# Optimization experiments

Measured on AMD Instinct MI355X. Metric: run time of the kernel, lower is better.

Reference implementation:

```python
import jax, jax.numpy as jnp
import numpy as np
from itertools import combinations

WAY = 5
TSS = 3  # temporal_set_size


def setup_inputs() -> dict:
    key = jax.random.key(0)
    k1, k2, k3 = jax.random.split(key, 3)
    n_support, n_queries, seq_len, D = 25, 400, 8, 2048
    d_out = D // 2
    support_set = jax.random.normal(k1, (n_support, seq_len, D), dtype=jnp.float32)
    queries = jax.random.normal(k2, (n_queries, seq_len, D), dtype=jnp.float32)
    support_labels = jnp.arange(n_support, dtype=jnp.int64) % WAY  # shot=5 per class
    W = jax.random.normal(k3, (d_out, TSS * D), dtype=jnp.float32) * 0.02
    b = jnp.zeros((d_out,), dtype=jnp.float32)
    return {"support_set": support_set, "support_labels": support_labels,
            "queries": queries, "W": W, "b": b}


def reference(support_set, support_labels, queries, W, b):
    # Dropout is identity at inference; omitted for determinism.
    n_s, seq_len, D = support_set.shape
    n_q = queries.shape[0]
    tup = jnp.asarray(list(combinations(range(seq_len), TSS)))  # [Tn, 3]
    Tn = tup.shape[0]
    # gather frame tuples and flatten: [N, Tn, 3*D]
    s = support_set[:, tup, :].reshape(n_s, Tn, TSS * D)
    q = queries[:, tup, :].reshape(n_q, Tn, TSS * D)
    # Linear + ReLU embedding
    qe = jax.nn.relu(q.reshape(n_q * Tn, TSS * D) @ W.T + b)          # [Q*Tn, d2]
    se = jax.nn.relu(s.reshape(n_s * Tn, TSS * D) @ W.T + b)
    se = se.reshape(n_s, Tn, -1)
    # group support by class (labels are static ints; shot per class is equal)
    order = jnp.argsort(support_labels, stable=True)                  # sorted by label
    cls_se = se[order.reshape(WAY, -1)].reshape(WAY, -1, se.shape[-1])  # [way, shot*Tn, d2]
    # pairwise Euclidean distances per class: ||q||^2 + ||s||^2 - 2 q.s
    q2 = jnp.sum(qe * qe, axis=-1)                                    # [Q*Tn]
    s2 = jnp.sum(cls_se * cls_se, axis=-1)                            # [way, shot*Tn]
    dots = jnp.einsum('qd,csd->cqs', qe, cls_se)                      # [way, Q*Tn, shot*Tn]
    dist = jnp.sqrt(jnp.maximum(q2[None, :, None] + s2[:, None, :] - 2.0 * dots, 0.0))
    min_dist = dist.min(axis=2).reshape(WAY, n_q, Tn)                 # min over class supports
    logits = -min_dist.mean(axis=2).T                                 # [n_q, way]
    return logits
```

## Files before the change

### kernel.cpp

```cpp
#include <hip/hip_runtime.h>
#include <math.h>

#define NSUP 25
#define NQ   400
#define SL   8
#define DIM  2048
#define DOUT 1024
#define WAY  5
#define TN   56
#define SHOT 5
#define QT   (NQ*TN)
#define STC  (SHOT*TN)
#define NFS  (NSUP*SL)
#define NFQ  (NQ*SL)
#define MF   (NFS+NFQ)
#define MFP  3584
#define PN   (3*DOUT)
#define NSE  1400
#define NSEP 1408

typedef __attribute__((ext_vector_type(8))) short short8;
typedef __attribute__((ext_vector_type(8))) int   int8v;
typedef __attribute__((ext_vector_type(4))) float f32x4;

#define GLOAD_LDS(g, l) __builtin_amdgcn_global_load_lds( \
    (const __attribute__((address_space(1))) unsigned*)(g), \
    (__attribute__((address_space(3))) unsigned*)(l), 16, 0, 0)

__device__ __forceinline__ unsigned short f2bf(float x) {
  unsigned u = __float_as_uint(x);
  u += 0x7fff + ((u >> 16) & 1);
  return (unsigned short)(u >> 16);
}
__device__ __forceinline__ float bf2f(unsigned short h) {
  return __uint_as_float(((unsigned)h) << 16);
}
__device__ __forceinline__ unsigned pk4_fp8(float a, float b, float c, float d) {
  unsigned p = __builtin_amdgcn_cvt_pk_fp8_f32(a, b, 0, false);
  p = __builtin_amdgcn_cvt_pk_fp8_f32(c, d, p, true);
  return p;
}
__device__ __forceinline__ float f8deq(unsigned b) {
  unsigned e = (b >> 3) & 15, m = b & 7;
  return e ? ldexpf((float)(8 + m), (int)e - 10) : ldexpf((float)m, -9);
}

__device__ __constant__ unsigned short TUP[TN] = {
  0x210,0x310,0x410,0x510,0x610,0x710,
  0x320,0x420,0x520,0x620,0x720,
  0x430,0x530,0x630,0x730,
  0x540,0x640,0x740,
  0x650,0x750,
  0x760,
  0x321,0x421,0x521,0x621,0x721,
  0x431,0x531,0x631,0x731,
  0x541,0x641,0x741,
  0x651,0x751,
  0x761,
  0x432,0x532,0x632,0x732,
  0x542,0x642,0x742,
  0x652,0x752,
  0x762,
  0x543,0x643,0x743,
  0x653,0x753,
  0x763,
  0x654,0x754,
  0x764,
  0x765
};

__global__ __launch_bounds__(256) void prep(
    const float* __restrict__ sup, const float* __restrict__ qry,
    const float* __restrict__ W,
    unsigned char* __restrict__ A8, unsigned char* __restrict__ W8,
    unsigned char* __restrict__ se8, float* __restrict__ s2,
    unsigned* __restrict__ pmin)
{
  int idx = blockIdx.x * 256 + threadIdx.x;
  {
    int e = idx * 4;
    int row = e >> 11, c = e & 2047;
    float4 v = make_float4(0.f, 0.f, 0.f, 0.f);
    if (row < NFS)      v = *(const float4*)(sup + (size_t)row * DIM + c);
    else if (row < MF)  v = *(const float4*)(qry + (size_t)(row - NFS) * DIM + c);
    *(unsigned*)(A8 + e) = pk4_fp8(v.x, v.y, v.z, v.w);
  }
  if (idx < PN*DIM/4) {
    int e = idx * 4;
    int n = e >> 11, c = e & 2047;
    const float4 v = *(const float4*)(W + (size_t)(n & 1023) * (3*DIM) + (n >> 10) * DIM + c);
    *(unsigned*)(W8 + e) = pk4_fp8(v.x*64.f, v.y*64.f, v.z*64.f, v.w*64.f);
  }
  if (idx < WAY * QT) pmin[idx] = 0x7F800000u;
  if (idx < (NSEP - NSE) * DOUT) se8[(size_t)NSE * DOUT + idx] = 0;
  if (idx < NSEP - NSE) s2[NSE + idx] = 0.f;
}

__device__ __forceinline__ void mfma_kloop_f8(
    const unsigned char* __restrict__ gA, const unsigned char* __restrict__ gB,
    int sa, int sb, int rowA0, int rowB0, int clampA,
    unsigned char* As, unsigned char* Bs,
    int w, int l, int nk, f32x4 acc[8][4])
{
  const int lrow = l >> 3;
  const int cswz = ((((l >> 1) & 3) ^ (lrow & 3)) * 2 + (l & 1)) * 16;
  unsigned offA[8], offB[4];
#pragma unroll
  for (int q = 0; q < 8; ++q)
    offA[q] = (unsigned)min(rowA0 + w*64 + q*8 + lrow, clampA) * sa + cswz;
#pragma unroll
  for (int q = 0; q < 4; ++q)
    offB[q] = (unsigned)(rowB0 + w*32 + q*8 + lrow) * sb + cswz;
  unsigned char* lA = As + (w*64) * 128;
  unsigned char* lB = Bs + (w*32) * 128;
  const int lane15 = l & 15, quad = l >> 4;
  const int wm = (w & 1) * 128, wn = (w >> 1) * 64;
  const int slot = (quad ^ (lane15 & 3)) * 32;

  int koff = 0;
  for (int kk = 0; kk < nk; ++kk, koff += 128) {
    __syncthreads();
#pragma unroll
    for (int q = 0; q < 8; ++q) GLOAD_LDS(gA + offA[q] + koff, lA + q*1024);
#pragma unroll
    for (int q = 0; q < 4; ++q) GLOAD_LDS(gB + offB[q] + koff, lB + q*1024);
    __syncthreads();
    int8v af[8];
#pragma unroll
    for (int i = 0; i < 8; ++i)
      af[i] = *(const int8v*)(As + (wm + i*16 + lane15)*128 + slot);
#pragma unroll
    for (int j = 0; j < 4; ++j) {
      int8v bf = *(const int8v*)(Bs + (wn + j*16 + lane15)*128 + slot);
#pragma unroll
      for (int i = 0; i < 8; ++i)
        acc[i][j] = __builtin_amdgcn_mfma_scale_f32_16x16x128_f8f6f4(
            af[i], bf, acc[i][j], 0, 0, 0, 0x7f7f7f7f, 0, 0x7f7f7f7f);
    }
  }
}

__global__ __launch_bounds__(256, 2) void gemm_embed_f8(
    const unsigned char* __restrict__ A8, const unsigned char* __restrict__ W8,
    unsigned short* __restrict__ P)
{
  __shared__ unsigned char As[256*128];
  __shared__ unsigned char Bs[128*128];
  int n = blockIdx.x;
  int g = n / 112, j = n % 112;
  const int bm = (j >> 3) * 256, bn = (g*8 + (j & 7)) * 128;
  const int tid = threadIdx.x, w = tid >> 6, l = tid & 63;
  const int lane15 = l & 15, quad = l >> 4;
  const int wm = (w & 1) * 128, wn = (w >> 1) * 64;

  f32x4 acc[8][4] = {};
  mfma_kloop_f8(A8, W8, DIM, DIM, bm, bn, MFP-1, As, Bs, w, l, DIM/128, acc);

#pragma unroll
  for (int i = 0; i < 8; ++i) {
#pragma unroll
    for (int r = 0; r < 4; ++r) {
      int row = bm + wm + i*16 + quad*4 + r;
      if (row < MF) {
#pragma unroll
        for (int j2 = 0; j2 < 4; ++j2) {
          int col = bn + wn + j2*16 + lane15;
          P[(size_t)row * PN + col] = f2bf(acc[i][j2][r] * 0.015625f);
        }
      }
    }
  }
}

__global__ __launch_bounds__(256) void assemble_seq(
    const unsigned short* __restrict__ P, const float* __restrict__ bias,
    unsigned char* __restrict__ qe8, float* __restrict__ q2,
    unsigned char* __restrict__ se8, float* __restrict__ s2)
{
  __shared__ unsigned short sP[SL * PN];
  const int b2 = blockIdx.x, b = b2 >> 1, half = b2 & 1;
  const int tid = threadIdx.x, w = tid >> 6, l = tid & 63;

  const size_t base = (size_t)b * SL * PN;
#pragma unroll
  for (int qi = 0; qi < 12; ++qi) {
    int off = (qi * 256 + tid) * 8;
    *(short8*)&sP[off] = *(const short8*)(P + base + off);
  }
  __syncthreads();

  float4 bbv[4];
#pragma unroll
  for (int c = 0; c < 4; ++c)
    bbv[c] = *(const float4*)&bias[l*4 + c*256];

  const bool is_sup = b < NSUP;
  unsigned char* E = is_sup ? se8 : qe8;
  float* nrm = is_sup ? s2 : q2;
  int row_base;
  if (is_sup) { int cc = b % WAY, kk = b / WAY; row_base = cc * STC + kk * TN; }
  else        { row_base = (b - NSUP) * TN; }

  const int t_end = half * 28 + 28;
  for (int t = half * 28 + w; t < t_end; t += 4) {
    unsigned int tp = TUP[t];
    int f0 = tp & 15, f1 = (tp >> 4) & 15, f2 = (tp >> 8) & 15;
    int row = row_base + t;
    float ssq = 0.f;
#pragma unroll
    for (int c = 0; c < 4; ++c) {
      int o = l*4 + c*256;
      ushort4 a = *(const ushort4*)&sP[f0*PN + o];
      ushort4 bq = *(const ushort4*)&sP[f1*PN + DOUT + o];
      ushort4 d = *(const ushort4*)&sP[f2*PN + 2*DOUT + o];
      float z0 = fmaxf(bf2f(a.x) + bf2f(bq.x) + bf2f(d.x) + bbv[c].x, 0.f);
      float z1 = fmaxf(bf2f(a.y) + bf2f(bq.y) + bf2f(d.y) + bbv[c].y, 0.f);
      float z2 = fmaxf(bf2f(a.z) + bf2f(bq.z) + bf2f(d.z) + bbv[c].z, 0.f);
      float z3 = fmaxf(bf2f(a.w) + bf2f(bq.w) + bf2f(d.w) + bbv[c].w, 0.f);
      unsigned pk = pk4_fp8(z0, z1, z2, z3);
      *(unsigned*)&E[(size_t)row * DOUT + o] = pk;
      float x0 = f8deq(pk & 255),         x1 = f8deq((pk >> 8) & 255);
      float x2 = f8deq((pk >> 16) & 255), x3 = f8deq(pk >> 24);
      ssq += x0*x0 + x1*x1 + x2*x2 + x3*x3;
    }
#pragma unroll
    for (int off = 1; off < 64; off <<= 1) ssq += __shfl_xor(ssq, off, 64);
    if (l == 0) nrm[row] = ssq;
  }
}

__global__ __launch_bounds__(256, 2) void gemm_dist_f8(
    const unsigned char* __restrict__ qe8, const unsigned char* __restrict__ se8,
    const float* __restrict__ q2, const float* __restrict__ s2,
    unsigned* __restrict__ pmin)
{
  __shared__ unsigned char As[256*128];
  __shared__ unsigned char Bs[128*128];
  int n = blockIdx.x;
  int x, y;
  if (n < 1008) { int g = n / 48, j = n % 48; y = g*8 + (j & 7); x = j >> 3; }
  else          { int m = n - 1008; y = 168 + m % 7; x = m / 7; }
  const int bm = x * 256;
  const int bn = y * 128;
  const int tid = threadIdx.x, w = tid >> 6, l = tid & 63;
  const int lane15 = l & 15, quad = l >> 4;
  const int wm = (w & 1) * 128, wn = (w >> 1) * 64;

  f32x4 acc[8][4] = {};
  mfma_kloop_f8(se8, qe8, DOUT, DOUT, bm, bn, NSEP-1, As, Bs, w, l, DOUT/128, acc);

  float s2v[8][4]; int clsv[8][4];
#pragma unroll
  for (int i = 0; i < 8; ++i)
#pragma unroll
    for (int r = 0; r < 4; ++r) {
      int sec = bm + wm + i*16 + quad*4 + r;
      s2v[i][r] = s2[min(sec, NSEP-1)];
      clsv[i][r] = sec / STC;
    }
#pragma unroll
  for (int i = 0; i < 8; ++i)
#pragma unroll
    for (int j = 0; j < 4; ++j)
#pragma unroll
      for (int r = 0; r < 4; ++r)
        acc[i][j][r] = fmaf(-2.f, acc[i][j][r], s2v[i][r]);

  float q2v[4];
#pragma unroll
  for (int j = 0; j < 4; ++j)
    q2v[j] = q2[bn + wn + j*16 + lane15];

  const int c_lo = (bm + wm) / STC;
  const int c_hi = min((bm + wm + 127) / STC, WAY - 1);
  for (int c = c_lo; c <= c_hi; ++c) {
#pragma unroll
    for (int j = 0; j < 4; ++j) {
      float mv = INFINITY;
#pragma unroll
      for (int i = 0; i < 8; ++i)
#pragma unroll
        for (int r = 0; r < 4; ++r)
          mv = fminf(mv, (clsv[i][r] == c) ? acc[i][j][r] : INFINITY);
      mv = fminf(mv, __shfl_xor(mv, 16, 64));
      mv = fminf(mv, __shfl_xor(mv, 32, 64));
      if (quad == 0) {
        float val = fmaxf(q2v[j] + mv, 0.f);
        atomicMin(&pmin[(size_t)c * QT + bn + wn + j*16 + lane15],
                  __float_as_uint(val));
      }
    }
  }
}

__global__ void finalize(const unsigned* __restrict__ pmin, float* __restrict__ out)
{
  int idx = blockIdx.x * blockDim.x + threadIdx.x;
  if (idx >= NQ * WAY) return;
  int i = idx / WAY, c = idx % WAY;
  float sum = 0.f;
  for (int t = 0; t < TN; ++t) {
    float v = __uint_as_float(pmin[(size_t)c * QT + i * TN + t]);
    sum += sqrtf(v);
  }
  out[i * WAY + c] = -sum * (1.f / (float)TN);
}

extern "C" void kernel_launch(void* const* d_in, const int* in_sizes, int n_in,
                              void* d_out, int out_size, void* d_ws, size_t ws_size,
                              hipStream_t stream) {
  const float* support = (const float*)d_in[0];
  const float* queries  = (const float*)d_in[2];
  const float* W        = (const float*)d_in[3];
  const float* bias     = (const float*)d_in[4];
  float* out = (float*)d_out;

  char* ws = (char*)d_ws;
  unsigned char* A8 = (unsigned char*)ws;           ws += (size_t)MFP * DIM;
  unsigned char* W8 = (unsigned char*)ws;           ws += (size_t)PN * DIM;
  unsigned short* P = (unsigned short*)ws;          ws += (size_t)MF * PN * 2;
  unsigned char* qe8 = (unsigned char*)ws;          ws += (size_t)QT * DOUT;
  unsigned char* se8 = (unsigned char*)ws;          ws += (size_t)NSEP * DOUT;
  float*         q2  = (float*)ws;                  ws += (size_t)QT * 4;
  float*         s2  = (float*)ws;                  ws += (size_t)NSEP * 4;
  unsigned*      pm  = (unsigned*)ws;

  prep<<<MFP*DIM/4/256, 256, 0, stream>>>(support, queries, W, A8, W8, se8, s2, pm);
  gemm_embed_f8<<<336, 256, 0, stream>>>(A8, W8, P);
  assemble_seq<<<2*(NSUP + NQ), 256, 0, stream>>>(P, bias, qe8, q2, se8, s2);
  gemm_dist_f8<<<1050, 256, 0, stream>>>(qe8, se8, q2, s2, pm);
  finalize<<<(NQ*WAY + 255)/256, 256, 0, stream>>>(pm, out);
}
```

Measured before the change: 201.2 us.

## Fuse frame-embedding GEMM with tuple assembly, dropping the bf16 intermediate buffer

Merges the frame-level embedding GEMM and the tuple-assembly kernel into one kernel. Each block computes a 64-frame by 128-output-column slice across all three weight segments, stages it as bf16 in LDS, then builds the ReLU'd fp8 tuple embeddings and partial squared norms directly. Norms are accumulated with atomics into buffers that prep now zeroes. This removes the global write and re-read of the intermediate P buffer and one kernel launch. The cost is a smaller GEMM tile with less reuse, plus per-row atomics. The fp8 dequantisation helper is also rewritten as bit manipulation instead of ldexpf.

```diff
diff --git a/kernel.cpp b/kernel.cpp
--- a/kernel.cpp
+++ b/kernel.cpp
@@ -14,6 +14,7 @@
 #define NFS  (NSUP*SL)
 #define NFQ  (NQ*SL)
 #define MF   (NFS+NFQ)
+#define NSEQ (NSUP+NQ)
 #define MFP  3584
 #define PN   (3*DOUT)
 #define NSE  1400
@@ -42,7 +43,9 @@
 }
 __device__ __forceinline__ float f8deq(unsigned b) {
   unsigned e = (b >> 3) & 15, m = b & 7;
-  return e ? ldexpf((float)(8 + m), (int)e - 10) : ldexpf((float)m, -9);
+  float n = __uint_as_float(((e + 120) << 23) | (m << 20));
+  float s = (float)m * 0.001953125f;
+  return e ? n : s;
 }
 
 __device__ __constant__ unsigned short TUP[TN] = {
@@ -74,7 +77,7 @@
     const float* __restrict__ W,
     unsigned char* __restrict__ A8, unsigned char* __restrict__ W8,
     unsigned char* __restrict__ se8, float* __restrict__ s2,
-    unsigned* __restrict__ pmin)
+    float* __restrict__ q2, unsigned* __restrict__ pmin)
 {
   int idx = blockIdx.x * 256 + threadIdx.x;
   {
@@ -93,7 +96,113 @@
   }
   if (idx < WAY * QT) pmin[idx] = 0x7F800000u;
   if (idx < (NSEP - NSE) * DOUT) se8[(size_t)NSE * DOUT + idx] = 0;
-  if (idx < NSEP - NSE) s2[NSE + idx] = 0.f;
+  if (idx < QT)   q2[idx] = 0.f;
+  if (idx < NSEP) s2[idx] = 0.f;
+}
+
+__global__ __launch_bounds__(256, 2) void embed_fused(
+    const unsigned char* __restrict__ A8, const unsigned char* __restrict__ W8,
+    const float* __restrict__ bias,
+    unsigned char* __restrict__ qe8, float* __restrict__ q2,
+    unsigned char* __restrict__ se8, float* __restrict__ s2)
+{
+  __shared__ __align__(16) unsigned char smem[57344];
+  unsigned char* As = smem;
+  unsigned char* Bs = smem + 8192;
+  unsigned short* sPb = (unsigned short*)smem;
+
+  const int bid = blockIdx.x;
+  const int ot = bid & 7, bs = bid >> 3;
+  const int bm = bs * 64;
+  const int tid = threadIdx.x, w = tid >> 6, l = tid & 63;
+  const int lane15 = l & 15, quad = l >> 4;
+  const int lrow = l >> 3;
+  const int cswz = ((((l >> 1) & 3) ^ (lrow & 3)) * 2 + (l & 1)) * 16;
+
+  unsigned offA[2], offB[12];
+#pragma unroll
+  for (int q = 0; q < 2; ++q)
+    offA[q] = (unsigned)min(bm + w*16 + q*8 + lrow, MF-1) * DIM + cswz;
+#pragma unroll
+  for (int m = 0; m < 12; ++m) {
+    int s = m >> 2, q = m & 3;
+    offB[m] = (unsigned)(s*1024 + ot*128 + w*32 + q*8 + lrow) * DIM + cswz;
+  }
+  const int slot = (quad ^ (lane15 & 3)) * 32;
+
+  f32x4 acc[4][6] = {};
+  int koff = 0;
+  for (int kk = 0; kk < 16; ++kk, koff += 128) {
+    __syncthreads();
+#pragma unroll
+    for (int q = 0; q < 2; ++q)
+      GLOAD_LDS(A8 + offA[q] + koff, As + (w*16)*128 + q*1024);
+#pragma unroll
+    for (int m = 0; m < 12; ++m) {
+      int s = m >> 2, q = m & 3;
+      GLOAD_LDS(W8 + offB[m] + koff, Bs + (s*128 + w*32)*128 + q*1024);
+    }
+    __syncthreads();
+    int8v af[4];
+#pragma unroll
+    for (int i = 0; i < 4; ++i)
+      af[i] = *(const int8v*)(As + (i*16 + lane15)*128 + slot);
+#pragma unroll
+    for (int j = 0; j < 6; ++j) {
+      int8v bf = *(const int8v*)(Bs + (w*96 + j*16 + lane15)*128 + slot);
+#pragma unroll
+      for (int i = 0; i < 4; ++i)
+        acc[i][j] = __builtin_amdgcn_mfma_scale_f32_16x16x128_f8f6f4(
+            af[i], bf, acc[i][j], 0, 0, 0, 0x7f7f7f7f, 0, 0x7f7f7f7f);
+    }
+  }
+
+  __syncthreads();
+#pragma unroll
+  for (int i = 0; i < 4; ++i)
+#pragma unroll
+    for (int j = 0; j < 6; ++j)
+#pragma unroll
+      for (int r = 0; r < 4; ++r)
+        sPb[(i*16 + quad*4 + r)*384 + (w*96 + j*16 + lane15)] =
+            f2bf(acc[i][j][r] * 0.015625f);
+  __syncthreads();
+
+  const int sl = 2*w + (l >> 5);
+  const int lc = l & 31;
+  const int seq = bs*8 + sl;
+  const int og = ot*128 + lc*4;
+  const float4 bb = *(const float4*)&bias[og];
+  const bool valid = seq < NSEQ;
+  const bool is_sup = seq < NSUP;
+  unsigned char* E = is_sup ? se8 : qe8;
+  float* nrm = is_sup ? s2 : q2;
+  int row_base = is_sup ? (seq % WAY) * STC + (seq / WAY) * TN
+                        : (seq - NSUP) * TN;
+  const unsigned short* base0 = sPb + sl * 8 * 384 + lc * 4;
+
+  for (int t = 0; t < TN; ++t) {
+    unsigned tp = TUP[t];
+    int f0 = tp & 15, f1 = (tp >> 4) & 15, f2 = (tp >> 8) & 15;
+    ushort4 a  = *(const ushort4*)(base0 + f0*384);
+    ushort4 bq = *(const ushort4*)(base0 + f1*384 + 128);
+    ushort4 d  = *(const ushort4*)(base0 + f2*384 + 256);
+    float z0 = fmaxf(bf2f(a.x) + bf2f(bq.x) + bf2f(d.x) + bb.x, 0.f);
+    float z1 = fmaxf(bf2f(a.y) + bf2f(bq.y) + bf2f(d.y) + bb.y, 0.f);
+    float z2 = fmaxf(bf2f(a.z) + bf2f(bq.z) + bf2f(d.z) + bb.z, 0.f);
+    float z3 = fmaxf(bf2f(a.w) + bf2f(bq.w) + bf2f(d.w) + bb.w, 0.f);
+    unsigned pk = pk4_fp8(z0, z1, z2, z3);
+    float x0 = f8deq(pk & 255),         x1 = f8deq((pk >> 8) & 255);
+    float x2 = f8deq((pk >> 16) & 255), x3 = f8deq(pk >> 24);
+    float ssq = x0*x0 + x1*x1 + x2*x2 + x3*x3;
+#pragma unroll
+    for (int off = 1; off < 32; off <<= 1) ssq += __shfl_xor(ssq, off, 64);
+    if (valid) {
+      int row = row_base + t;
+      *(unsigned*)&E[(size_t)row * DOUT + og] = pk;
+      if (lc == 0) atomicAdd(&nrm[row], ssq);
+    }
+  }
 }
 
 __device__ __forceinline__ void mfma_kloop_f8(
@@ -137,95 +246,6 @@
         acc[i][j] = __builtin_amdgcn_mfma_scale_f32_16x16x128_f8f6f4(
             af[i], bf, acc[i][j], 0, 0, 0, 0x7f7f7f7f, 0, 0x7f7f7f7f);
     }
-  }
-}
-
-__global__ __launch_bounds__(256, 2) void gemm_embed_f8(
-    const unsigned char* __restrict__ A8, const unsigned char* __restrict__ W8,
-    unsigned short* __restrict__ P)
-{
-  __shared__ unsigned char As[256*128];
-  __shared__ unsigned char Bs[128*128];
-  int n = blockIdx.x;
-  int g = n / 112, j = n % 112;
-  const int bm = (j >> 3) * 256, bn = (g*8 + (j & 7)) * 128;
-  const int tid = threadIdx.x, w = tid >> 6, l = tid & 63;
-  const int lane15 = l & 15, quad = l >> 4;
-  const int wm = (w & 1) * 128, wn = (w >> 1) * 64;
-
-  f32x4 acc[8][4] = {};
-  mfma_kloop_f8(A8, W8, DIM, DIM, bm, bn, MFP-1, As, Bs, w, l, DIM/128, acc);
-
-#pragma unroll
-  for (int i = 0; i < 8; ++i) {
-#pragma unroll
-    for (int r = 0; r < 4; ++r) {
-      int row = bm + wm + i*16 + quad*4 + r;
-      if (row < MF) {
-#pragma unroll
-        for (int j2 = 0; j2 < 4; ++j2) {
-          int col = bn + wn + j2*16 + lane15;
-          P[(size_t)row * PN + col] = f2bf(acc[i][j2][r] * 0.015625f);
-        }
-      }
-    }
-  }
-}
-
-__global__ __launch_bounds__(256) void assemble_seq(
-    const unsigned short* __restrict__ P, const float* __restrict__ bias,
-    unsigned char* __restrict__ qe8, float* __restrict__ q2,
-    unsigned char* __restrict__ se8, float* __restrict__ s2)
-{
-  __shared__ unsigned short sP[SL * PN];
-  const int b2 = blockIdx.x, b = b2 >> 1, half = b2 & 1;
-  const int tid = threadIdx.x, w = tid >> 6, l = tid & 63;
-
-  const size_t base = (size_t)b * SL * PN;
-#pragma unroll
-  for (int qi = 0; qi < 12; ++qi) {
-    int off = (qi * 256 + tid) * 8;
-    *(short8*)&sP[off] = *(const short8*)(P + base + off);
-  }
-  __syncthreads();
-
-  float4 bbv[4];
-#pragma unroll
-  for (int c = 0; c < 4; ++c)
-    bbv[c] = *(const float4*)&bias[l*4 + c*256];
-
-  const bool is_sup = b < NSUP;
-  unsigned char* E = is_sup ? se8 : qe8;
-  float* nrm = is_sup ? s2 : q2;
-  int row_base;
-  if (is_sup) { int cc = b % WAY, kk = b / WAY; row_base = cc * STC + kk * TN; }
-  else        { row_base = (b - NSUP) * TN; }
-
-  const int t_end = half * 28 + 28;
-  for (int t = half * 28 + w; t < t_end; t += 4) {
-    unsigned int tp = TUP[t];
-    int f0 = tp & 15, f1 = (tp >> 4) & 15, f2 = (tp >> 8) & 15;
-    int row = row_base + t;
-    float ssq = 0.f;
-#pragma unroll
-    for (int c = 0; c < 4; ++c) {
-      int o = l*4 + c*256;
-      ushort4 a = *(const ushort4*)&sP[f0*PN + o];
-      ushort4 bq = *(const ushort4*)&sP[f1*PN + DOUT + o];
-      ushort4 d = *(const ushort4*)&sP[f2*PN + 2*DOUT + o];
-      float z0 = fmaxf(bf2f(a.x) + bf2f(bq.x) + bf2f(d.x) + bbv[c].x, 0.f);
-      float z1 = fmaxf(bf2f(a.y) + bf2f(bq.y) + bf2f(d.y) + bbv[c].y, 0.f);
-      float z2 = fmaxf(bf2f(a.z) + bf2f(bq.z) + bf2f(d.z) + bbv[c].z, 0.f);
-      float z3 = fmaxf(bf2f(a.w) + bf2f(bq.w) + bf2f(d.w) + bbv[c].w, 0.f);
-      unsigned pk = pk4_fp8(z0, z1, z2, z3);
-      *(unsigned*)&E[(size_t)row * DOUT + o] = pk;
-      float x0 = f8deq(pk & 255),         x1 = f8deq((pk >> 8) & 255);
-      float x2 = f8deq((pk >> 16) & 255), x3 = f8deq(pk >> 24);
-      ssq += x0*x0 + x1*x1 + x2*x2 + x3*x3;
-    }
-#pragma unroll
-    for (int off = 1; off < 64; off <<= 1) ssq += __shfl_xor(ssq, off, 64);
-    if (l == 0) nrm[row] = ssq;
   }
 }
 
@@ -318,16 +338,14 @@
   char* ws = (char*)d_ws;
   unsigned char* A8 = (unsigned char*)ws;           ws += (size_t)MFP * DIM;
   unsigned char* W8 = (unsigned char*)ws;           ws += (size_t)PN * DIM;
-  unsigned short* P = (unsigned short*)ws;          ws += (size_t)MF * PN * 2;
   unsigned char* qe8 = (unsigned char*)ws;          ws += (size_t)QT * DOUT;
   unsigned char* se8 = (unsigned char*)ws;          ws += (size_t)NSEP * DOUT;
   float*         q2  = (float*)ws;                  ws += (size_t)QT * 4;
   float*         s2  = (float*)ws;                  ws += (size_t)NSEP * 4;
   unsigned*      pm  = (unsigned*)ws;
 
-  prep<<<MFP*DIM/4/256, 256, 0, stream>>>(support, queries, W, A8, W8, se8, s2, pm);
-  gemm_embed_f8<<<336, 256, 0, stream>>>(A8, W8, P);
-  assemble_seq<<<2*(NSUP + NQ), 256, 0, stream>>>(P, bias, qe8, q2, se8, s2);
+  prep<<<MFP*DIM/4/256, 256, 0, stream>>>(support, queries, W, A8, W8, se8, s2, q2, pm);
+  embed_fused<<<432, 256, 0, stream>>>(A8, W8, bias, qe8, q2, se8, s2);
   gemm_dist_f8<<<1050, 256, 0, stream>>>(qe8, se8, q2, s2, pm);
   finalize<<<(NQ*WAY + 255)/256, 256, 0, stream>>>(pm, out);
 }
```

Result: slower. 212.1 us (+5.4%).
